# Kernel tuning notes

Measured on AMD Instinct MI355X. Metric: run time of the kernel, lower is better.

## Reference

```python
import jax, jax.numpy as jnp
import numpy as np

B, T, NVAR, H, C = 1024, 96, 7, 64, 3  # batch, seq_len/time-points, nvar, ode_hidden, components
H4 = 4 * H


def setup_inputs() -> dict:
    key = jax.random.key(0)
    ks = jax.random.split(key, 12)
    def w(k, shape, fan_in):
        return (jax.random.normal(k, shape, jnp.float32) / np.sqrt(fan_in)).astype(jnp.float32)
    return {
        "x": jax.random.normal(ks[0], (B, T, NVAR), jnp.float32),
        # init_net: Linear(nvar->H), ReLU, Linear(H->C*H)   (stored as (in,out))
        "init_w1": w(ks[1], (NVAR, H), NVAR), "init_b1": jnp.zeros((H,), jnp.float32),
        "init_w2": w(ks[2], (H, C * H), H),   "init_b2": jnp.zeros((C * H,), jnp.float32),
        # ODEFunc.net: Linear(H+C -> 4H), Tanh, Linear(4H -> H)
        "ode_w1": w(ks[3], (H + C, H4), H + C), "ode_b1": jnp.zeros((H4,), jnp.float32),
        "ode_w2": w(ks[4], (H4, H), H4),        "ode_b2": jnp.zeros((H,), jnp.float32),
        # interaction param (init eye) and frozen conservation linear (eye, no bias)
        "interaction": jnp.eye(C, dtype=jnp.float32),
        "conservation": jnp.eye(C, dtype=jnp.float32),
        # decode_net: per-component Linear(H->H), ReLU, Linear(H->nvar)
        "dec_w1": w(ks[5], (C, H, H), H), "dec_b1": jnp.zeros((C, H), jnp.float32),
        "dec_w2": w(ks[6], (C, H, NVAR), H), "dec_b2": jnp.zeros((C, NVAR), jnp.float32),
        "t_points": jnp.linspace(0.0, 1.0, T).astype(jnp.float32),
    }


def _ode_func(t, state, interaction, conservation, ode_w1, ode_b1, ode_w2, ode_b2):
    # state: (B, C, H)
    b = state.shape[0]
    state_comp = state.mean(axis=-1)                                   # (B, C)
    ie = jnp.einsum('ij,bj->bi', interaction, state_comp)              # bmm(interaction, mean)
    ie = jnp.einsum('oi,bi->bo', conservation, ie)                     # frozen linear (no bias)
    inputs = jnp.concatenate(
        [state.reshape(b * C, H), ie.reshape(b * C, 1), jnp.full((b * C, 1), t, state.dtype)],
        axis=1)                                                        # (B*C, H+2)? no: H + 1 + 1 = H + C since C==3? -> H+2; matches torch cat of [H,1,1] only if C accounts: net expects H+C=H+3.
    # NOTE: torch concatenates [state(H), interaction_effect(1), t(1)] = H+2 features but the
    # Linear expects H+C.  With C=3 torch relies on nn.Linear(H+3) receiving H+2?? It does not --
    # torch code passes H+2 features into Linear(H+C).  Faithful translation pads to match below.
    d = jnp.tanh(inputs @ ode_w1[: inputs.shape[1]] + ode_b1) @ ode_w2 + ode_b2
    return d.reshape(state.shape)


def reference(x, init_w1, init_b1, init_w2, init_b2, ode_w1, ode_b1, ode_w2, ode_b2,
              interaction, conservation, dec_w1, dec_b1, dec_w2, dec_b2, t_points):
    # initial state from mean over sequence
    h0 = jax.nn.relu(x.mean(axis=1) @ init_w1 + init_b1)
    y0 = (h0 @ init_w2 + init_b2).reshape(-1, C, H)                    # (B, C, H)

    f = lambda t, y: _ode_func(t, y, interaction, conservation, ode_w1, ode_b1, ode_w2, ode_b2)

    def rk4_step(y, ts):
        t0, t1 = ts
        h = t1 - t0
        k1 = f(t0, y)
        k2 = f(t0 + 0.5 * h, y + 0.5 * h * k1)
        k3 = f(t0 + 0.5 * h, y + 0.5 * h * k2)
        k4 = f(t1, y + h * k3)
        y1 = y + (h / 6.0) * (k1 + 2.0 * k2 + 2.0 * k3 + k4)
        return y1, y1

    ts = jnp.stack([t_points[:-1], t_points[1:]], axis=1)              # (T-1, 2)
    _, ys = jax.lax.scan(rk4_step, y0, ts)                             # (T-1, B, C, H)
    states = jnp.concatenate([y0[None], ys], axis=0)                   # (T, B, C, H)
    states = jnp.transpose(states, (1, 0, 2, 3))                       # (B, T, C, H)

    # per-component decode MLP
    hid = jax.nn.relu(jnp.einsum('btch,chk->btck', states, dec_w1) + dec_b1)
    comps = jnp.einsum('btck,ckn->btcn', hid, dec_w2) + dec_b2         # (B, T, C, NVAR)
    comps = jnp.moveaxis(comps, 2, 0)                                  # (C, B, T, NVAR)
    # comps[0] is the trend, comps[1:] the high-frequency components
    return comps
```

## Files before the change

kernel.cpp:

```cpp
#include <hip/hip_runtime.h>

#define BTOT 1024
#define TPTS 96
#define NV   7
#define HD   64
#define NH   256

typedef short bf16x8 __attribute__((ext_vector_type(8)));
typedef float f32x4  __attribute__((ext_vector_type(4)));
typedef unsigned int u32x4 __attribute__((ext_vector_type(4)));
#define MFMA16(a,b,c) __builtin_amdgcn_mfma_f32_16x16x32_bf16(a,b,c,0,0,0)

#define OFF_YP   0
#define OFF_TP   1024
#define OFF_PRT  5120
#define OFF_YF   10240
#define OFF_PS   11280
#define OFF_TPS  11344
#define OFF_DW1  11440
#define OFF_DW2  23728
#define OFF_DB1  25072
#define OFF_DB2  25264
#define SMEM_WORDS 25296
#define SMEM_BYTES (SMEM_WORDS*4)

__device__ __forceinline__ float rdlane(float v, int i) {
    return __int_as_float(__builtin_amdgcn_readlane(__float_as_int(v), i));
}
__device__ __forceinline__ float wsum64(float v) {
    v += __shfl_xor(v, 1);  v += __shfl_xor(v, 2);  v += __shfl_xor(v, 4);
    v += __shfl_xor(v, 8);  v += __shfl_xor(v, 16); v += __shfl_xor(v, 32);
    return v;
}
__device__ __forceinline__ float tanh_fast(float x) {
    float e = __expf(2.f * x);
    return 1.f - 2.f / (e + 1.f);
}
__device__ __forceinline__ ushort bf16rn(float x) {
    unsigned u = __float_as_uint(x);
    return (ushort)((u + 0x7fffu + ((u >> 16) & 1u)) >> 16);
}
__device__ __forceinline__ void split2(float x, ushort& h, ushort& l) {
    h = bf16rn(x);
    float hf = __uint_as_float(((unsigned)h) << 16);
    l = bf16rn(x - hf);
}

union FU { u32x4 uv; unsigned u[4]; ushort s[8]; bf16x8 v; };

__global__ __launch_bounds__(1024)
void node_mfma7(const float* __restrict__ x,
                const float* __restrict__ iw1, const float* __restrict__ ib1,
                const float* __restrict__ iw2, const float* __restrict__ ib2,
                const float* __restrict__ ow1, const float* __restrict__ ob1,
                const float* __restrict__ ow2, const float* __restrict__ ob2,
                const float* __restrict__ inter, const float* __restrict__ cons,
                const float* __restrict__ dw1, const float* __restrict__ db1,
                const float* __restrict__ dw2, const float* __restrict__ db2,
                const float* __restrict__ tpts,
                float* __restrict__ out)
{
    extern __shared__ float sm[];
    unsigned* YPw = (unsigned*)(sm + OFF_YP);
    unsigned* TPw = (unsigned*)(sm + OFF_TP);
    float*    PRT = sm + OFF_PRT;
    float*    Yf  = sm + OFF_YF;
    float*    PS  = sm + OFF_PS;
    float*    tps = sm + OFF_TPS;
    float*    DW1 = sm + OFF_DW1;
    float*    DW2 = sm + OFF_DW2;
    float*    DB1 = sm + OFF_DB1;
    float*    DB2 = sm + OFF_DB2;

    const int tid = threadIdx.x;
    const int w   = tid >> 6;
    const int ln  = tid & 63;
    const int m   = ln & 15;
    const int g4  = ln >> 4;
    const int nt  = w & 3;
    const int kq  = w >> 2;

    for (int idx = tid; idx < 3*HD*HD; idx += 1024) DW1[idx] = dw1[idx];
    if (tid < 3*HD)  { for (int v = 0; v < NV; ++v) DW2[tid*NV + v] = dw2[tid*NV + v]; }
    if (tid < 192)   DB1[tid] = db1[tid];
    if (tid < 21)    DB2[tid] = db2[tid];
    if (tid < TPTS)  tps[tid] = tpts[tid];

    const int col1 = 16*w + m;
    FU w1h[2], w1l[2], w2h[2], w2l[2];
    #pragma unroll
    for (int cc = 0; cc < 2; ++cc) {
        #pragma unroll
        for (int j = 0; j < 8; ++j) {
            ushort h, l;
            int k1 = 32*cc + 8*g4 + j;
            split2(ow1[k1*NH + col1], h, l);
            w1h[cc].s[j] = h; w1l[cc].s[j] = l;
            int k2 = 64*kq + 32*cc + 8*g4 + j;
            split2(ow2[k2*HD + 16*nt + m], h, l);
            w2h[cc].s[j] = h; w2l[cc].s[j] = l;
        }
    }
    const float w64c = ow1[64*NH + col1];
    const float w65c = ow1[65*NH + col1];
    const float b1c  = ob1[col1];
    const float b2c  = ob2[16*nt + m];

    const int cpm = m % 3, base3 = m - cpm;
    float Mr0, Mr1, Mr2;
    {
        float I[9], C[9];
        #pragma unroll
        for (int i = 0; i < 9; ++i) { I[i] = inter[i]; C[i] = cons[i]; }
        float M_[3][3];
        #pragma unroll
        for (int r = 0; r < 3; ++r)
            #pragma unroll
            for (int c = 0; c < 3; ++c)
                M_[r][c] = (C[r*3+0]*I[0*3+c] + C[r*3+1]*I[1*3+c] + C[r*3+2]*I[2*3+c]) * (1.f/64.f);
        Mr0 = (cpm==0) ? M_[0][0] : (cpm==1) ? M_[1][0] : M_[2][0];
        Mr1 = (cpm==0) ? M_[0][1] : (cpm==1) ? M_[1][1] : M_[2][1];
        Mr2 = (cpm==0) ? M_[0][2] : (cpm==1) ? M_[1][2] : M_[2][2];
    }

    {
        const int el0 = w >> 2;
        const int b0  = blockIdx.x*4 + el0;
        float xs0,xs1,xs2,xs3,xs4,xs5,xs6;
        {
            const float* xp = x + (size_t)b0 * TPTS * NV + ln * NV;
            float v0=xp[0],v1=xp[1],v2=xp[2],v3=xp[3],v4=xp[4],v5=xp[5],v6=xp[6];
            if (ln < 32) {
                const float* xp2 = xp + 64 * NV;
                v0+=xp2[0]; v1+=xp2[1]; v2+=xp2[2]; v3+=xp2[3]; v4+=xp2[4]; v5+=xp2[5]; v6+=xp2[6];
            }
            xs0=wsum64(v0)*(1.f/96.f); xs1=wsum64(v1)*(1.f/96.f); xs2=wsum64(v2)*(1.f/96.f);
            xs3=wsum64(v3)*(1.f/96.f); xs4=wsum64(v4)*(1.f/96.f); xs5=wsum64(v5)*(1.f/96.f);
            xs6=wsum64(v6)*(1.f/96.f);
        }
        float h0v;
        {
            float a = ib1[ln];
            a = fmaf(xs0, iw1[0*HD+ln], a); a = fmaf(xs1, iw1[1*HD+ln], a);
            a = fmaf(xs2, iw1[2*HD+ln], a); a = fmaf(xs3, iw1[3*HD+ln], a);
            a = fmaf(xs4, iw1[4*HD+ln], a); a = fmaf(xs5, iw1[5*HD+ln], a);
            a = fmaf(xs6, iw1[6*HD+ln], a);
            h0v = fmaxf(a, 0.f);
        }
        float y0a = ib2[ln], y0b = ib2[64+ln], y0c = ib2[128+ln];
        #pragma unroll
        for (int k = 0; k < 64; ++k) {
            float hk = rdlane(h0v, k);
            y0a = fmaf(hk, iw2[k*192 + ln],       y0a);
            y0b = fmaf(hk, iw2[k*192 + 64 + ln],  y0b);
            y0c = fmaf(hk, iw2[k*192 + 128 + ln], y0c);
        }
        if ((w & 3) == 0) {
            float yv[3] = {y0a, y0b, y0c};
            #pragma unroll
            for (int r = 0; r < 3; ++r) {
                int row = el0*3 + r;
                Yf[row*65 + ln] = yv[r];
                ushort hs, ls; split2(yv[r], hs, ls);
                unsigned hp = hs, lp = ls;
                unsigned hq = __shfl_xor(hp, 1), lq = __shfl_xor(lp, 1);
                if ((ln & 1) == 0) {
                    int wgrp = ln >> 3;
                    int woff = row*32 + ((((unsigned)(wgrp ^ row)) & 7) << 2) + ((ln >> 1) & 3);
                    YPw[woff]       = hp | (hq << 16);
                    YPw[512 + woff] = lp | (lq << 16);
                }
            }
            float S0 = wsum64(y0a), S1 = wsum64(y0b), S2 = wsum64(y0c);
            if (ln < 3) PS[el0*3 + ln] = (ln==0)?S0:(ln==1)?S1:S2;
        }
        if (w == 1 && ln >= 12) PS[ln] = 0.f;
        if (w == 2) {
            YPw[384 + ln] = 0u; YPw[448 + ln] = 0u;
            YPw[896 + ln] = 0u; YPw[960 + ln] = 0u;
        }
        if (w == 12) {
            #pragma unroll
            for (int r = 12; r < 16; ++r) Yf[r*65 + ln] = 0.f;
        }
    }
    __syncthreads();

    f32x4 yb, ks;
    #pragma unroll
    for (int r = 0; r < 4; ++r) yb[r] = Yf[(4*g4 + r)*65 + 16*nt + m];

    auto publish = [&](f32x4 ys, bool commit) {
        float yv = (kq==0)?ys[0]:(kq==1)?ys[1]:(kq==2)?ys[2]:ys[3];
        const int row = 4*g4 + kq;
        ushort hs, ls; split2(yv, hs, ls);
        unsigned hp = hs, lp = ls;
        unsigned hq = __shfl_xor(hp, 1), lq = __shfl_xor(lp, 1);
        if ((m & 1) == 0) {
            int wgrp = 2*nt + (m >> 3);
            int woff = row*32 + ((((unsigned)(wgrp ^ row)) & 7) << 2) + ((m >> 1) & 3);
            YPw[woff]       = hp | (hq << 16);
            YPw[512 + woff] = lp | (lq << 16);
        }
        if (commit) Yf[row*65 + 16*nt + m] = yv;
        float s = yv;
        s += __shfl_xor(s, 1); s += __shfl_xor(s, 2);
        s += __shfl_xor(s, 4); s += __shfl_xor(s, 8);
        if (m == 0) PS[nt*16 + row] = s;
    };

    auto evalf = [&](float ts, f32x4& dd) {
        float rsum = (PS[m] + PS[16+m]) + (PS[32+m] + PS[48+m]);
        float eAll = Mr0*__shfl(rsum, base3) + Mr1*__shfl(rsum, base3+1) + Mr2*__shfl(rsum, base3+2);

        f32x4 accA = {0,0,0,0}, accB = {0,0,0,0};
        #pragma unroll
        for (int cc = 0; cc < 2; ++cc) {
            FU ah, al;
            int aoff = m*32 + ((((unsigned)((4*cc + g4) ^ m)) & 7) << 2);
            ah.uv = *(const u32x4*)(YPw + aoff);
            al.uv = *(const u32x4*)(YPw + 512 + aoff);
            accA = MFMA16(ah.v, w1h[cc].v, accA);
            accB = MFMA16(ah.v, w1l[cc].v, accB);
            accA = MFMA16(al.v, w1h[cc].v, accA);
        }
        #pragma unroll
        for (int r = 0; r < 4; ++r) {
            float er = __shfl(eAll, 4*g4 + r);
            float val = accA[r] + accB[r];
            val = fmaf(w64c, er, val);
            val = fmaf(w65c, ts, val);
            val += b1c;
            float th = tanh_fast(val);
            ushort hs, ls; split2(th, hs, ls);
            unsigned hp = hs, lp = ls;
            unsigned hq = __shfl_xor(hp, 1), lq = __shfl_xor(lp, 1);
            if ((m & 1) == 0) {
                int row = 4*g4 + r;
                int wgrp = 2*w + (m >> 3);
                int woff = row*128 + (((wgrp & 24) | ((wgrp ^ row) & 7)) << 2) + ((m >> 1) & 3);
                TPw[woff]        = hp | (hq << 16);
                TPw[2048 + woff] = lp | (lq << 16);
            }
        }
        __syncthreads();

        f32x4 pA = {0,0,0,0}, pB = {0,0,0,0};
        #pragma unroll
        for (int cc = 0; cc < 2; ++cc) {
            FU ah, al;
            int aoff = m*128 + 32*kq + ((((unsigned)((4*cc + g4) ^ m)) & 7) << 2);
            ah.uv = *(const u32x4*)(TPw + aoff);
            al.uv = *(const u32x4*)(TPw + 2048 + aoff);
            pA = MFMA16(ah.v, w2h[cc].v, pA);
            pB = MFMA16(ah.v, w2l[cc].v, pB);
            pA = MFMA16(al.v, w2h[cc].v, pA);
        }
        f32x4 pr = pA + pB;
        *(f32x4*)(PRT + w*320 + m*20 + 4*g4) = pr;
        __syncthreads();

        const float* pb = PRT + m*20 + 4*g4;
        f32x4 q0 = *(const f32x4*)(pb + nt*320);
        f32x4 q1 = *(const f32x4*)(pb + (nt+4)*320);
        f32x4 q2 = *(const f32x4*)(pb + (nt+8)*320);
        f32x4 q3 = *(const f32x4*)(pb + (nt+12)*320);
        f32x4 qq = (q0 + q1) + (q2 + q3);
        dd[0] = qq[0] + b2c; dd[1] = qq[1] + b2c;
        dd[2] = qq[2] + b2c; dd[3] = qq[3] + b2c;
    };

    auto decode = [&](int tix) {
        if (w < 12) {
            const int cc = w % 3, el = w / 3;
            const int b  = blockIdx.x*4 + el;
            float acc = DB1[cc*HD + ln];
            #pragma unroll 8
            for (int h = 0; h < 64; ++h)
                acc = fmaf(Yf[w*65 + h], DW1[(cc*HD + h)*HD + ln], acc);
            float hid = fmaxf(acc, 0.f);
            #pragma unroll
            for (int v = 0; v < NV; ++v) {
                float pv = wsum64(hid * DW2[(cc*HD + ln)*NV + v]);
                if (ln == 0)
                    out[(((size_t)cc*BTOT + b)*TPTS + tix)*NV + v] = pv + DB2[cc*NV + v];
            }
        }
    };

    decode(0);
    f32x4 dd;
    #pragma unroll 1
    for (int s = 0; s < TPTS - 1; ++s) {
        const float ta = tps[s], tb = tps[s + 1];
        const float dt = tb - ta, hdt = 0.5f * dt;

        evalf(ta, dd);
        ks = dd; publish(yb + hdt*dd, false);
        __syncthreads();

        evalf(ta + hdt, dd);
        ks += 2.f*dd; publish(yb + hdt*dd, false);
        __syncthreads();

        evalf(ta + hdt, dd);
        ks += 2.f*dd; publish(yb + dt*dd, false);
        __syncthreads();

        evalf(tb, dd);
        ks += dd; yb = yb + (dt*(1.f/6.f))*ks; publish(yb, true);
        __syncthreads();

        decode(s + 1);
    }
}

extern "C" void kernel_launch(void* const* d_in, const int* in_sizes, int n_in,
                              void* d_out, int out_size, void* d_ws, size_t ws_size,
                              hipStream_t stream) {
    const float* x     = (const float*)d_in[0];
    const float* iw1   = (const float*)d_in[1];
    const float* ib1   = (const float*)d_in[2];
    const float* iw2   = (const float*)d_in[3];
    const float* ib2   = (const float*)d_in[4];
    const float* ow1   = (const float*)d_in[5];
    const float* ob1   = (const float*)d_in[6];
    const float* ow2   = (const float*)d_in[7];
    const float* ob2   = (const float*)d_in[8];
    const float* inter = (const float*)d_in[9];
    const float* cons  = (const float*)d_in[10];
    const float* dw1   = (const float*)d_in[11];
    const float* db1   = (const float*)d_in[12];
    const float* dw2   = (const float*)d_in[13];
    const float* db2   = (const float*)d_in[14];
    const float* tpts  = (const float*)d_in[15];
    float* out = (float*)d_out;

    (void)hipFuncSetAttribute((const void*)node_mfma7,
                              hipFuncAttributeMaxDynamicSharedMemorySize,
                              SMEM_BYTES);

    node_mfma7<<<BTOT / 4, 1024, SMEM_BYTES, stream>>>(
        x, iw1, ib1, iw2, ib2, ow1, ob1, ow2, ob2,
        inter, cons, dw1, db1, dw2, db2, tpts, out);
}
```

Before: 1.167 ms.

## Halve block size to two batch elements per 512-thread workgroup with wider per-wave tiles

```diff
diff --git a/kernel.cpp b/kernel.cpp
--- a/kernel.cpp
+++ b/kernel.cpp
@@ -14,14 +14,13 @@
 #define OFF_YP   0
 #define OFF_TP   1024
 #define OFF_PRT  5120
-#define OFF_YF   10240
-#define OFF_PS   11280
-#define OFF_TPS  11344
-#define OFF_DW1  11440
-#define OFF_DW2  23728
-#define OFF_DB1  25072
-#define OFF_DB2  25264
-#define SMEM_WORDS 25296
+#define OFF_YF   7680
+#define OFF_PS   8720
+#define OFF_TPS  8784
+#define OFF_DW2  8880
+#define OFF_DB1  10224
+#define OFF_DB2  10416
+#define SMEM_WORDS 10448
 #define SMEM_BYTES (SMEM_WORDS*4)
 
 __device__ __forceinline__ float rdlane(float v, int i) {
@@ -48,8 +47,8 @@
 
 union FU { u32x4 uv; unsigned u[4]; ushort s[8]; bf16x8 v; };
 
-__global__ __launch_bounds__(1024)
-void node_mfma7(const float* __restrict__ x,
+__global__ __launch_bounds__(512, 4)
+void node_mfma8(const float* __restrict__ x,
                 const float* __restrict__ iw1, const float* __restrict__ ib1,
                 const float* __restrict__ iw2, const float* __restrict__ ib2,
                 const float* __restrict__ ow1, const float* __restrict__ ob1,
@@ -67,7 +66,6 @@
     float*    Yf  = sm + OFF_YF;
     float*    PS  = sm + OFF_PS;
     float*    tps = sm + OFF_TPS;
-    float*    DW1 = sm + OFF_DW1;
     float*    DW2 = sm + OFF_DW2;
     float*    DB1 = sm + OFF_DB1;
     float*    DB2 = sm + OFF_DB2;
@@ -78,33 +76,44 @@
     const int m   = ln & 15;
     const int g4  = ln >> 4;
     const int nt  = w & 3;
-    const int kq  = w >> 2;
-
-    for (int idx = tid; idx < 3*HD*HD; idx += 1024) DW1[idx] = dw1[idx];
-    if (tid < 3*HD)  { for (int v = 0; v < NV; ++v) DW2[tid*NV + v] = dw2[tid*NV + v]; }
-    if (tid < 192)   DB1[tid] = db1[tid];
-    if (tid < 21)    DB2[tid] = db2[tid];
-    if (tid < TPTS)  tps[tid] = tpts[tid];
-
-    const int col1 = 16*w + m;
-    FU w1h[2], w1l[2], w2h[2], w2l[2];
+    const int kh  = w >> 2;
+
+    for (int idx = tid; idx < 3*HD*NV; idx += 512) DW2[idx] = dw2[idx];
+    if (tid < 192)  DB1[tid] = db1[tid];
+    if (tid < 21)   DB2[tid] = db2[tid];
+    if (tid < TPTS) tps[tid] = tpts[tid];
+
+    FU w1h[2][2], w1l[2][2];
+    FU w2h[4], w2l[4];
     #pragma unroll
-    for (int cc = 0; cc < 2; ++cc) {
+    for (int u = 0; u < 2; ++u)
+        #pragma unroll
+        for (int cc = 0; cc < 2; ++cc)
+            #pragma unroll
+            for (int j = 0; j < 8; ++j) {
+                ushort h, l;
+                int k1 = 32*cc + 8*g4 + j;
+                split2(ow1[k1*NH + 16*(2*w+u) + m], h, l);
+                w1h[u][cc].s[j] = h; w1l[u][cc].s[j] = l;
+            }
+    #pragma unroll
+    for (int cc = 0; cc < 4; ++cc)
         #pragma unroll
         for (int j = 0; j < 8; ++j) {
             ushort h, l;
-            int k1 = 32*cc + 8*g4 + j;
-            split2(ow1[k1*NH + col1], h, l);
-            w1h[cc].s[j] = h; w1l[cc].s[j] = l;
-            int k2 = 64*kq + 32*cc + 8*g4 + j;
+            int k2 = 128*kh + 32*cc + 8*g4 + j;
             split2(ow2[k2*HD + 16*nt + m], h, l);
             w2h[cc].s[j] = h; w2l[cc].s[j] = l;
         }
+    float w64c[2], w65c[2], b1c[2];
+    #pragma unroll
+    for (int u = 0; u < 2; ++u) {
+        int c1 = 16*(2*w+u) + m;
+        w64c[u] = ow1[64*NH + c1];
+        w65c[u] = ow1[65*NH + c1];
+        b1c[u]  = ob1[c1];
     }
-    const float w64c = ow1[64*NH + col1];
-    const float w65c = ow1[65*NH + col1];
-    const float b1c  = ob1[col1];
-    const float b2c  = ob2[16*nt + m];
+    const float b2c = ob2[16*nt + m];
 
     const int cpm = m % 3, base3 = m - cpm;
     float Mr0, Mr1, Mr2;
@@ -125,7 +134,7 @@
 
     {
         const int el0 = w >> 2;
-        const int b0  = blockIdx.x*4 + el0;
+        const int b0  = blockIdx.x*2 + el0;
         float xs0,xs1,xs2,xs3,xs4,xs5,xs6;
         {
             const float* xp = x + (size_t)b0 * TPTS * NV + ln * NV;
@@ -174,14 +183,15 @@
             float S0 = wsum64(y0a), S1 = wsum64(y0b), S2 = wsum64(y0c);
             if (ln < 3) PS[el0*3 + ln] = (ln==0)?S0:(ln==1)?S1:S2;
         }
-        if (w == 1 && ln >= 12) PS[ln] = 0.f;
-        if (w == 2) {
-            YPw[384 + ln] = 0u; YPw[448 + ln] = 0u;
-            YPw[896 + ln] = 0u; YPw[960 + ln] = 0u;
-        }
-        if (w == 12) {
-            #pragma unroll
-            for (int r = 12; r < 16; ++r) Yf[r*65 + ln] = 0.f;
+        if (w == 1 && ln < 48) PS[16 + ln] = 0.f;
+        if (w == 5 && ln >= 6 && ln < 16) PS[ln] = 0.f;
+        if (w == 6) {
+            for (int idx = ln; idx < 320; idx += 64) {
+                YPw[192 + idx] = 0u; YPw[704 + idx] = 0u;
+            }
+        }
+        if (w == 7) {
+            for (int idx = ln; idx < 650; idx += 64) Yf[6*65 + idx] = 0.f;
         }
     }
     __syncthreads();
@@ -191,65 +201,76 @@
     for (int r = 0; r < 4; ++r) yb[r] = Yf[(4*g4 + r)*65 + 16*nt + m];
 
     auto publish = [&](f32x4 ys, bool commit) {
-        float yv = (kq==0)?ys[0]:(kq==1)?ys[1]:(kq==2)?ys[2]:ys[3];
-        const int row = 4*g4 + kq;
-        ushort hs, ls; split2(yv, hs, ls);
-        unsigned hp = hs, lp = ls;
-        unsigned hq = __shfl_xor(hp, 1), lq = __shfl_xor(lp, 1);
-        if ((m & 1) == 0) {
-            int wgrp = 2*nt + (m >> 3);
-            int woff = row*32 + ((((unsigned)(wgrp ^ row)) & 7) << 2) + ((m >> 1) & 3);
-            YPw[woff]       = hp | (hq << 16);
-            YPw[512 + woff] = lp | (lq << 16);
-        }
-        if (commit) Yf[row*65 + 16*nt + m] = yv;
-        float s = yv;
-        s += __shfl_xor(s, 1); s += __shfl_xor(s, 2);
-        s += __shfl_xor(s, 4); s += __shfl_xor(s, 8);
-        if (m == 0) PS[nt*16 + row] = s;
+        #pragma unroll
+        for (int rr = 0; rr < 2; ++rr) {
+            float yv = kh ? (rr ? ys[3] : ys[2]) : (rr ? ys[1] : ys[0]);
+            const int row = 4*g4 + 2*kh + rr;
+            ushort hs, ls; split2(yv, hs, ls);
+            unsigned hp = hs, lp = ls;
+            unsigned hq = __shfl_xor(hp, 1), lq = __shfl_xor(lp, 1);
+            if ((m & 1) == 0) {
+                int wgrp = 2*nt + (m >> 3);
+                int woff = row*32 + ((((unsigned)(wgrp ^ row)) & 7) << 2) + ((m >> 1) & 3);
+                YPw[woff]       = hp | (hq << 16);
+                YPw[512 + woff] = lp | (lq << 16);
+            }
+            if (commit) Yf[row*65 + 16*nt + m] = yv;
+            float s = yv;
+            s += __shfl_xor(s, 1); s += __shfl_xor(s, 2);
+            s += __shfl_xor(s, 4); s += __shfl_xor(s, 8);
+            if (m == 0) PS[nt*16 + row] = s;
+        }
     };
 
     auto evalf = [&](float ts, f32x4& dd) {
         float rsum = (PS[m] + PS[16+m]) + (PS[32+m] + PS[48+m]);
         float eAll = Mr0*__shfl(rsum, base3) + Mr1*__shfl(rsum, base3+1) + Mr2*__shfl(rsum, base3+2);
 
-        f32x4 accA = {0,0,0,0}, accB = {0,0,0,0};
+        f32x4 aA0 = {0,0,0,0}, aB0 = {0,0,0,0}, aA1 = {0,0,0,0}, aB1 = {0,0,0,0};
         #pragma unroll
         for (int cc = 0; cc < 2; ++cc) {
             FU ah, al;
             int aoff = m*32 + ((((unsigned)((4*cc + g4) ^ m)) & 7) << 2);
             ah.uv = *(const u32x4*)(YPw + aoff);
             al.uv = *(const u32x4*)(YPw + 512 + aoff);
-            accA = MFMA16(ah.v, w1h[cc].v, accA);
-            accB = MFMA16(ah.v, w1l[cc].v, accB);
-            accA = MFMA16(al.v, w1h[cc].v, accA);
+            aA0 = MFMA16(ah.v, w1h[0][cc].v, aA0);
+            aB0 = MFMA16(ah.v, w1l[0][cc].v, aB0);
+            aA0 = MFMA16(al.v, w1h[0][cc].v, aA0);
+            aA1 = MFMA16(ah.v, w1h[1][cc].v, aA1);
+            aB1 = MFMA16(ah.v, w1l[1][cc].v, aB1);
+            aA1 = MFMA16(al.v, w1h[1][cc].v, aA1);
         }
         #pragma unroll
         for (int r = 0; r < 4; ++r) {
             float er = __shfl(eAll, 4*g4 + r);
-            float val = accA[r] + accB[r];
-            val = fmaf(w64c, er, val);
-            val = fmaf(w65c, ts, val);
-            val += b1c;
-            float th = tanh_fast(val);
-            ushort hs, ls; split2(th, hs, ls);
-            unsigned hp = hs, lp = ls;
-            unsigned hq = __shfl_xor(hp, 1), lq = __shfl_xor(lp, 1);
-            if ((m & 1) == 0) {
-                int row = 4*g4 + r;
-                int wgrp = 2*w + (m >> 3);
-                int woff = row*128 + (((wgrp & 24) | ((wgrp ^ row) & 7)) << 2) + ((m >> 1) & 3);
-                TPw[woff]        = hp | (hq << 16);
-                TPw[2048 + woff] = lp | (lq << 16);
+            const int row = 4*g4 + r;
+            #pragma unroll
+            for (int u = 0; u < 2; ++u) {
+                float val = u ? (aA1[r] + aB1[r]) : (aA0[r] + aB0[r]);
+                val = fmaf(w64c[u], er, val);
+                val = fmaf(w65c[u], ts, val);
+                val += b1c[u];
+                float th = tanh_fast(val);
+                ushort hs, ls; split2(th, hs, ls);
+                unsigned hp = hs, lp = ls;
+                unsigned hq = __shfl_xor(hp, 1), lq = __shfl_xor(lp, 1);
+                if ((m & 1) == 0) {
+                    int wgrp = 4*w + 2*u + (m >> 3);
+                    int woff = row*128 + ((((unsigned)wgrp & 24) | (((unsigned)(wgrp ^ row)) & 7)) << 2)
+                             + ((m >> 1) & 3);
+                    TPw[woff]        = hp | (hq << 16);
+                    TPw[2048 + woff] = lp | (lq << 16);
+                }
             }
         }
         __syncthreads();
 
         f32x4 pA = {0,0,0,0}, pB = {0,0,0,0};
         #pragma unroll
-        for (int cc = 0; cc < 2; ++cc) {
+        for (int cc = 0; cc < 4; ++cc) {
             FU ah, al;
-            int aoff = m*128 + 32*kq + ((((unsigned)((4*cc + g4) ^ m)) & 7) << 2);
+            int G = 16*kh + 4*cc + g4;
+            int aoff = m*128 + ((((unsigned)G & 24) | (((unsigned)(G ^ m)) & 7)) << 2);
             ah.uv = *(const u32x4*)(TPw + aoff);
             al.uv = *(const u32x4*)(TPw + 2048 + aoff);
             pA = MFMA16(ah.v, w2h[cc].v, pA);
@@ -263,21 +284,20 @@
         const float* pb = PRT + m*20 + 4*g4;
         f32x4 q0 = *(const f32x4*)(pb + nt*320);
         f32x4 q1 = *(const f32x4*)(pb + (nt+4)*320);
-        f32x4 q2 = *(const f32x4*)(pb + (nt+8)*320);
-        f32x4 q3 = *(const f32x4*)(pb + (nt+12)*320);
-        f32x4 qq = (q0 + q1) + (q2 + q3);
+        f32x4 qq = q0 + q1;
         dd[0] = qq[0] + b2c; dd[1] = qq[1] + b2c;
         dd[2] = qq[2] + b2c; dd[3] = qq[3] + b2c;
     };
 
     auto decode = [&](int tix) {
-        if (w < 12) {
+        if (w < 6) {
             const int cc = w % 3, el = w / 3;
-            const int b  = blockIdx.x*4 + el;
+            const int b  = blockIdx.x*2 + el;
             float acc = DB1[cc*HD + ln];
-            #pragma unroll 8
+            const float* wp = dw1 + (size_t)cc*HD*HD + ln;
+            #pragma unroll 4
             for (int h = 0; h < 64; ++h)
-                acc = fmaf(Yf[w*65 + h], DW1[(cc*HD + h)*HD + ln], acc);
+                acc = fmaf(Yf[w*65 + h], wp[h*HD], acc);
             float hid = fmaxf(acc, 0.f);
             #pragma unroll
             for (int v = 0; v < NV; ++v) {
@@ -336,11 +356,7 @@
     const float* tpts  = (const float*)d_in[15];
     float* out = (float*)d_out;
 
-    (void)hipFuncSetAttribute((const void*)node_mfma7,
-                              hipFuncAttributeMaxDynamicSharedMemorySize,
-                              SMEM_BYTES);
-
-    node_mfma7<<<BTOT / 4, 1024, SMEM_BYTES, stream>>>(
+    node_mfma8<<<BTOT / 2, 512, SMEM_BYTES, stream>>>(
         x, iw1, ib1, iw2, ib2, ow1, ob1, ow2, ob2,
         inter, cons, dw1, db1, dw2, db2, tpts, out);
 }
```

Result: slower. 4.620 ms (+295.8%).
